# Kernel tuning notes

Hardware: AMD Instinct MI355X
Metric: run time of the kernel (lower is better)

## Reference

```python
import jax, jax.numpy as jnp
import numpy as np

B, S, H = 4, 512, 1024
E, K, I = 8, 2, 2048

def setup_inputs() -> dict:
    key = jax.random.key(0)
    k1, k2, k3, k4, k5 = jax.random.split(key, 5)
    scale_h = 1.0 / np.sqrt(H)
    scale_i = 1.0 / np.sqrt(I)
    return {
        "hidden_states": jax.random.normal(k1, (B, S, H), dtype=jnp.float32),
        "router_w": jax.random.normal(k2, (E, H), dtype=jnp.float32) * scale_h,
        "w_gate": jax.random.normal(k3, (E, H, I), dtype=jnp.float32) * scale_h,
        "w_up": jax.random.normal(k4, (E, H, I), dtype=jnp.float32) * scale_h,
        "w_down": jax.random.normal(k5, (E, I, H), dtype=jnp.float32) * scale_i,
    }

def reference(hidden_states, router_w, w_gate, w_up, w_down):
    b, s, h = hidden_states.shape
    x = hidden_states.reshape(-1, h)              # [T, H] tokens
    T = x.shape[0]

    # ---- RouterTopK: fp32 linear -> softmax over all experts -> top-k ----
    router_logits = x.astype(jnp.float32) @ router_w.T          # [T, E]
    probs = jax.nn.softmax(router_logits, axis=-1)               # [T, E]
    top_vals, top_idx = jax.lax.top_k(probs, K)                  # [T, K]

    # normalize_top_k_affinities (norm_topk_prob=True)
    top_vals = top_vals / jnp.sum(top_vals, axis=-1, keepdims=True)

    # scatter normalized affinities into a dense [T, E] combine matrix
    aff = jnp.zeros((T, E), dtype=x.dtype).at[jnp.arange(T)[:, None], top_idx].set(top_vals.astype(x.dtype))

    # ---- ExpertMLPs: GLU (swiglu) per expert, combine weighted by affinity ----
    # Dense-per-expert computation; non-selected experts contribute 0 via aff.
    gate = jnp.einsum('th,ehi->eti', x, w_gate)                  # [E, T, I]
    up = jnp.einsum('th,ehi->eti', x, w_up)                      # [E, T, I]
    act = jax.nn.silu(gate) * up                                 # [E, T, I]
    expert_out = jnp.einsum('eti,eih->eth', act, w_down)         # [E, T, H]
    out = jnp.einsum('eth,te->th', expert_out, aff)              # [T, H]

    # _reduce_output: all-reduce over TP/world group -> identity single-device
    return out.reshape(b, s, h)
```

## Files before the change

### kernel.cpp

```cpp
#include <hip/hip_runtime.h>
#include <hip/hip_bf16.h>

#define T_TOK 2048
#define H_DIM 1024
#define E_N   8
#define I_DIM 2048

#define NT_MAX 40
#define MAX_SLOTS 5120

typedef unsigned short u16;
typedef unsigned int   u32;
typedef __bf16 bf16_t;
typedef bf16_t bf16x8 __attribute__((ext_vector_type(8)));
typedef u16    u16x8  __attribute__((ext_vector_type(8)));
typedef float  f32x4  __attribute__((ext_vector_type(4)));

#define MFMA __builtin_amdgcn_mfma_f32_16x16x32_bf16

__device__ __forceinline__ u16 bfbits(float f) {
    bf16_t b = (bf16_t)f;
    return __builtin_bit_cast(u16, b);
}

__device__ __forceinline__ int bt_off(int n, int kb) {
    return n * 72 + ((kb ^ ((n >> 2) & 7)) << 3);
}

__global__ __launch_bounds__(64) void router_k(
    const float* __restrict__ x, const float* __restrict__ rw,
    int* __restrict__ cnt, int* __restrict__ tok, float* __restrict__ wts,
    u16* __restrict__ xbf)
{
    int t = blockIdx.x;
    int lane = threadIdx.x;
    const float* xr = x + (size_t)t * H_DIM;
    u16* xbr = xbf + (size_t)t * H_DIM;

    float acc[E_N];
#pragma unroll
    for (int e = 0; e < E_N; e++) acc[e] = 0.f;
    for (int j = 0; j < H_DIM / 64; j++) {
        float xv = xr[lane + 64 * j];
        xbr[lane + 64 * j] = bfbits(xv);
#pragma unroll
        for (int e = 0; e < E_N; e++)
            acc[e] += xv * rw[e * H_DIM + lane + 64 * j];
    }
#pragma unroll
    for (int e = 0; e < E_N; e++) {
        float v = acc[e];
        for (int off = 32; off; off >>= 1) v += __shfl_xor(v, off);
        acc[e] = v;
    }
    if (lane == 0) {
        int i0 = 0; float m0 = acc[0];
#pragma unroll
        for (int e = 1; e < E_N; e++) if (acc[e] > m0) { m0 = acc[e]; i0 = e; }
        int i1 = -1; float m1 = -INFINITY;
#pragma unroll
        for (int e = 0; e < E_N; e++) if (e != i0 && acc[e] > m1) { m1 = acc[e]; i1 = e; }
        float w0 = 1.f / (1.f + expf(m1 - m0));
        float w1 = 1.f - w0;
        int p0 = atomicAdd(&cnt[i0], 1);
        tok[i0 * T_TOK + p0] = t; wts[i0 * T_TOK + p0] = w0;
        int p1 = atomicAdd(&cnt[i1], 1);
        tok[i1 * T_TOK + p1] = t; wts[i1 * T_TOK + p1] = w1;
    }
}

__global__ void prefix_k(const int* __restrict__ cnt, int* __restrict__ offs_pad,
                         int* __restrict__ tile_e, int* __restrict__ tile_row0,
                         int* __restrict__ ntiles)
{
    if (threadIdx.x == 0) {
        int s = 0, nt = 0;
        for (int e = 0; e < E_N; e++) {
            offs_pad[e] = s;
            int c = cnt[e];
            int t = (c + 127) >> 7;
            for (int i = 0; i < t; i++) { tile_e[nt] = e; tile_row0[nt] = i * 128; nt++; }
            s += t * 128;
        }
        offs_pad[E_N] = s;
        *ntiles = nt;
    }
}

__global__ __launch_bounds__(256, 2) void gateup_k(
    const u16* __restrict__ xbf, const float* __restrict__ wg, const float* __restrict__ wu,
    const int* __restrict__ cnt, const int* __restrict__ offs_pad,
    const int* __restrict__ tile_e, const int* __restrict__ tile_row0,
    const int* __restrict__ ntiles, const int* __restrict__ tok,
    u16* __restrict__ act)
{
    int q = gridDim.x >> 3;
    int phys = blockIdx.x;
    int logical = (phys & 7) * q + (phys >> 3);
    int tb = logical % NT_MAX;
    int n0 = (logical / NT_MAX) * 128;
    if (tb >= *ntiles) return;
    int e = tile_e[tb], row0 = tile_row0[tb];
    int cntE = cnt[e];
    int slot0 = offs_pad[e] + row0;

    __shared__ u16 BT[2][2][128 * 72];

    int tid = threadIdx.x;
    int lane = tid & 63, wid = tid >> 6;
    int wm = wid >> 1, wn = wid & 1;
    int l15 = lane & 15, lg = lane >> 4;

    const u16* arow[4];
#pragma unroll
    for (int mf = 0; mf < 4; mf++) {
        int rr = row0 + wm * 64 + mf * 16 + l15;
        int rc = rr < cntE ? rr : cntE - 1;
        arow[mf] = xbf + (size_t)tok[e * T_TOK + rc] * H_DIM;
    }

    int nq = tid & 31;
    int kb = tid >> 5;
    int sn = nq * 4;

    const float* gptr = wg + ((size_t)e * H_DIM + kb * 8) * I_DIM + n0 + sn;
    const float* uptr = wu + ((size_t)e * H_DIM + kb * 8) * I_DIM + n0 + sn;

    float4 vg[8], vu[8];
#pragma unroll
    for (int i = 0; i < 8; i++) {
        vg[i] = *reinterpret_cast<const float4*>(gptr + (size_t)i * I_DIM);
        vu[i] = *reinterpret_cast<const float4*>(uptr + (size_t)i * I_DIM);
    }

    f32x4 accg[4][4], accu[4][4];
#pragma unroll
    for (int a = 0; a < 4; a++)
#pragma unroll
        for (int b = 0; b < 4; b++) { accg[a][b] = (f32x4)0.f; accu[a][b] = (f32x4)0.f; }

    for (int k0 = 0; k0 < H_DIM; k0 += 64) {
        int buf = (k0 >> 6) & 1;
#pragma unroll
        for (int c = 0; c < 4; c++) {
            u16x8 p;
#pragma unroll
            for (int i = 0; i < 8; i++) {
                float f = (c == 0) ? vg[i].x : (c == 1) ? vg[i].y : (c == 2) ? vg[i].z : vg[i].w;
                p[i] = bfbits(f);
            }
            *reinterpret_cast<u16x8*>(&BT[buf][0][bt_off(sn + c, kb)]) = p;
        }
#pragma unroll
        for (int c = 0; c < 4; c++) {
            u16x8 p;
#pragma unroll
            for (int i = 0; i < 8; i++) {
                float f = (c == 0) ? vu[i].x : (c == 1) ? vu[i].y : (c == 2) ? vu[i].z : vu[i].w;
                p[i] = bfbits(f);
            }
            *reinterpret_cast<u16x8*>(&BT[buf][1][bt_off(sn + c, kb)]) = p;
        }
        if (k0 + 64 < H_DIM) {
#pragma unroll
            for (int i = 0; i < 8; i++) {
                vg[i] = *reinterpret_cast<const float4*>(gptr + (size_t)(k0 + 64 + i) * I_DIM);
                vu[i] = *reinterpret_cast<const float4*>(uptr + (size_t)(k0 + 64 + i) * I_DIM);
            }
        }
        __syncthreads();

#pragma unroll
        for (int ks = 0; ks < 2; ks++) {
            bf16x8 af[4];
#pragma unroll
            for (int mf = 0; mf < 4; mf++)
                af[mf] = *reinterpret_cast<const bf16x8*>(arow[mf] + k0 + ks * 32 + lg * 8);
            int kbr = ks * 4 + lg;
#pragma unroll
            for (int nf = 0; nf < 4; nf++) {
                int c = wn * 64 + nf * 16 + l15;
                bf16x8 bg = *reinterpret_cast<const bf16x8*>(&BT[buf][0][bt_off(c, kbr)]);
                bf16x8 bu = *reinterpret_cast<const bf16x8*>(&BT[buf][1][bt_off(c, kbr)]);
#pragma unroll
                for (int mf = 0; mf < 4; mf++) {
                    accg[mf][nf] = MFMA(af[mf], bg, accg[mf][nf], 0, 0, 0);
                    accu[mf][nf] = MFMA(af[mf], bu, accu[mf][nf], 0, 0, 0);
                }
            }
        }
    }

#pragma unroll
    for (int mf = 0; mf < 4; mf++)
#pragma unroll
        for (int j = 0; j < 4; j++) {
            int rl = wm * 64 + mf * 16 + lg * 4 + j;
            bool valid = (row0 + rl) < cntE;
            size_t base = (size_t)(slot0 + rl) * I_DIM + n0;
#pragma unroll
            for (int nf = 0; nf < 4; nf++) {
                float g = accg[mf][nf][j];
                float u = accu[mf][nf][j];
                float a = valid ? (g / (1.f + expf(-g))) * u : 0.f;
                act[base + wn * 64 + nf * 16 + l15] = bfbits(a);
            }
        }
}

__global__ __launch_bounds__(256, 2) void down_k(
    const u16* __restrict__ act, const float* __restrict__ wd,
    const int* __restrict__ cnt, const int* __restrict__ offs_pad,
    const int* __restrict__ tile_e, const int* __restrict__ tile_row0,
    const int* __restrict__ ntiles, const int* __restrict__ tok,
    const float* __restrict__ wts, float* __restrict__ out)
{
    int q = gridDim.x >> 3;
    int phys = blockIdx.x;
    int logical = (phys & 7) * q + (phys >> 3);
    int tb = logical % NT_MAX;
    int h0 = (logical / NT_MAX) * 128;
    if (tb >= *ntiles) return;
    int e = tile_e[tb], row0 = tile_row0[tb];
    int cntE = cnt[e];
    int slot0 = offs_pad[e] + row0;

    __shared__ u16 BT[2][128 * 72];

    int tid = threadIdx.x;
    int lane = tid & 63, wid = tid >> 6;
    int wm = wid >> 1, wn = wid & 1;
    int l15 = lane & 15, lg = lane >> 4;

    const u16* arow[4];
#pragma unroll
    for (int mf = 0; mf < 4; mf++)
        arow[mf] = act + (size_t)(slot0 + wm * 64 + mf * 16 + l15) * I_DIM;

    int nq = tid & 31;
    int kb = tid >> 5;
    int sn = nq * 4;

    const float* dptr = wd + ((size_t)e * I_DIM + kb * 8) * H_DIM + h0 + sn;

    float4 vd[8];
#pragma unroll
    for (int i = 0; i < 8; i++)
        vd[i] = *reinterpret_cast<const float4*>(dptr + (size_t)i * H_DIM);

    f32x4 acc[4][4];
#pragma unroll
    for (int a = 0; a < 4; a++)
#pragma unroll
        for (int b = 0; b < 4; b++) acc[a][b] = (f32x4)0.f;

    for (int k0 = 0; k0 < I_DIM; k0 += 64) {
        int buf = (k0 >> 6) & 1;
#pragma unroll
        for (int c = 0; c < 4; c++) {
            u16x8 p;
#pragma unroll
            for (int i = 0; i < 8; i++) {
                float f = (c == 0) ? vd[i].x : (c == 1) ? vd[i].y : (c == 2) ? vd[i].z : vd[i].w;
                p[i] = bfbits(f);
            }
            *reinterpret_cast<u16x8*>(&BT[buf][bt_off(sn + c, kb)]) = p;
        }
        if (k0 + 64 < I_DIM) {
#pragma unroll
            for (int i = 0; i < 8; i++)
                vd[i] = *reinterpret_cast<const float4*>(dptr + (size_t)(k0 + 64 + i) * H_DIM);
        }
        __syncthreads();

#pragma unroll
        for (int ks = 0; ks < 2; ks++) {
            bf16x8 af[4];
#pragma unroll
            for (int mf = 0; mf < 4; mf++)
                af[mf] = *reinterpret_cast<const bf16x8*>(arow[mf] + k0 + ks * 32 + lg * 8);
            int kbr = ks * 4 + lg;
#pragma unroll
            for (int nf = 0; nf < 4; nf++) {
                int c = wn * 64 + nf * 16 + l15;
                bf16x8 bfr = *reinterpret_cast<const bf16x8*>(&BT[buf][bt_off(c, kbr)]);
#pragma unroll
                for (int mf = 0; mf < 4; mf++)
                    acc[mf][nf] = MFMA(af[mf], bfr, acc[mf][nf], 0, 0, 0);
            }
        }
    }

#pragma unroll
    for (int mf = 0; mf < 4; mf++)
#pragma unroll
        for (int j = 0; j < 4; j++) {
            int rl = wm * 64 + mf * 16 + lg * 4 + j;
            int gr = row0 + rl;
            if (gr < cntE) {
                float w = wts[e * T_TOK + gr];
                int t   = tok[e * T_TOK + gr];
                size_t base = (size_t)t * H_DIM + h0;
#pragma unroll
                for (int nf = 0; nf < 4; nf++)
                    atomicAdd(&out[base + wn * 64 + nf * 16 + l15], acc[mf][nf][j] * w);
            }
        }
}

extern "C" void kernel_launch(void* const* d_in, const int* in_sizes, int n_in,
                              void* d_out, int out_size, void* d_ws, size_t ws_size,
                              hipStream_t stream)
{
    const float* x  = (const float*)d_in[0];
    const float* rw = (const float*)d_in[1];
    const float* wg = (const float*)d_in[2];
    const float* wu = (const float*)d_in[3];
    const float* wd = (const float*)d_in[4];
    float* out = (float*)d_out;

    char* ws = (char*)d_ws;
    int*   cnt       = (int*)(ws);
    int*   ntiles    = (int*)(ws + 32);
    int*   offs_pad  = (int*)(ws + 64);
    int*   tile_e    = (int*)(ws + 256);
    int*   tile_row0 = (int*)(ws + 512);
    int*   tok       = (int*)(ws + 64 * 1024);
    float* wts       = (float*)(ws + 128 * 1024);
    u16*   xbf       = (u16*)(ws + 256 * 1024);
    u16*   act       = (u16*)(ws + 4608 * 1024);

    size_t need = 4608ull * 1024 + (size_t)MAX_SLOTS * I_DIM * 2;
    if (ws_size < need) return;

    hipMemsetAsync(cnt, 0, 32, stream);
    hipMemsetAsync(out, 0, (size_t)T_TOK * H_DIM * sizeof(float), stream);

    router_k<<<T_TOK, 64, 0, stream>>>(x, rw, cnt, tok, wts, xbf);
    prefix_k<<<1, 64, 0, stream>>>(cnt, offs_pad, tile_e, tile_row0, ntiles);
    gateup_k<<<NT_MAX * (I_DIM / 128), 256, 0, stream>>>(
        xbf, wg, wu, cnt, offs_pad, tile_e, tile_row0, ntiles, tok, act);
    down_k<<<NT_MAX * (H_DIM / 128), 256, 0, stream>>>(
        act, wd, cnt, offs_pad, tile_e, tile_row0, ntiles, tok, wts, out);
}
```

Before: 245.7 us.

## Halve GEMM N-tiles and split-K the down projection to raise parallelism

Gate/up GEMM tiles shrink from 128 to 64 output columns, and each half of the block now loads either gate or up weights instead of every thread loading both. The down projection also uses 64-column tiles and splits the K dimension in two, relying on the existing atomicAdd accumulation. Together these give many more blocks, plus higher launch-bounds occupancy hints, to fill the GPU's CUs when expert tiles are few. The cost is more redundant A-operand (activation) reads and twice as many atomic adds to the output.

```diff
diff --git a/kernel.cpp b/kernel.cpp
--- a/kernel.cpp
+++ b/kernel.cpp
@@ -87,7 +87,7 @@
     }
 }
 
-__global__ __launch_bounds__(256, 2) void gateup_k(
+__global__ __launch_bounds__(256, 3) void gateup_k(
     const u16* __restrict__ xbf, const float* __restrict__ wg, const float* __restrict__ wu,
     const int* __restrict__ cnt, const int* __restrict__ offs_pad,
     const int* __restrict__ tile_e, const int* __restrict__ tile_row0,
@@ -98,13 +98,13 @@
     int phys = blockIdx.x;
     int logical = (phys & 7) * q + (phys >> 3);
     int tb = logical % NT_MAX;
-    int n0 = (logical / NT_MAX) * 128;
+    int n0 = (logical / NT_MAX) * 64;
     if (tb >= *ntiles) return;
     int e = tile_e[tb], row0 = tile_row0[tb];
     int cntE = cnt[e];
     int slot0 = offs_pad[e] + row0;
 
-    __shared__ u16 BT[2][2][128 * 72];
+    __shared__ u16 BT[2][2][64 * 72];
 
     int tid = threadIdx.x;
     int lane = tid & 63, wid = tid >> 6;
@@ -119,26 +119,25 @@
         arow[mf] = xbf + (size_t)tok[e * T_TOK + rc] * H_DIM;
     }
 
-    int nq = tid & 31;
-    int kb = tid >> 5;
-    int sn = nq * 4;
-
-    const float* gptr = wg + ((size_t)e * H_DIM + kb * 8) * I_DIM + n0 + sn;
-    const float* uptr = wu + ((size_t)e * H_DIM + kb * 8) * I_DIM + n0 + sn;
-
-    float4 vg[8], vu[8];
-#pragma unroll
-    for (int i = 0; i < 8; i++) {
-        vg[i] = *reinterpret_cast<const float4*>(gptr + (size_t)i * I_DIM);
-        vu[i] = *reinterpret_cast<const float4*>(uptr + (size_t)i * I_DIM);
-    }
-
-    f32x4 accg[4][4], accu[4][4];
+    int mat  = tid >> 7;
+    int tid7 = tid & 127;
+    int kb   = tid7 >> 4;
+    int sn   = (tid7 & 15) * 4;
+
+    const float* wptr = (mat ? wu : wg) + ((size_t)e * H_DIM + kb * 8) * I_DIM + n0 + sn;
+
+    float4 v[8];
+#pragma unroll
+    for (int i = 0; i < 8; i++)
+        v[i] = *reinterpret_cast<const float4*>(wptr + (size_t)i * I_DIM);
+
+    f32x4 accg[4][2], accu[4][2];
 #pragma unroll
     for (int a = 0; a < 4; a++)
 #pragma unroll
-        for (int b = 0; b < 4; b++) { accg[a][b] = (f32x4)0.f; accu[a][b] = (f32x4)0.f; }
-
+        for (int b = 0; b < 2; b++) { accg[a][b] = (f32x4)0.f; accu[a][b] = (f32x4)0.f; }
+
+#pragma unroll 2
     for (int k0 = 0; k0 < H_DIM; k0 += 64) {
         int buf = (k0 >> 6) & 1;
 #pragma unroll
@@ -146,27 +145,15 @@
             u16x8 p;
 #pragma unroll
             for (int i = 0; i < 8; i++) {
-                float f = (c == 0) ? vg[i].x : (c == 1) ? vg[i].y : (c == 2) ? vg[i].z : vg[i].w;
+                float f = (c == 0) ? v[i].x : (c == 1) ? v[i].y : (c == 2) ? v[i].z : v[i].w;
                 p[i] = bfbits(f);
             }
-            *reinterpret_cast<u16x8*>(&BT[buf][0][bt_off(sn + c, kb)]) = p;
-        }
-#pragma unroll
-        for (int c = 0; c < 4; c++) {
-            u16x8 p;
-#pragma unroll
-            for (int i = 0; i < 8; i++) {
-                float f = (c == 0) ? vu[i].x : (c == 1) ? vu[i].y : (c == 2) ? vu[i].z : vu[i].w;
-                p[i] = bfbits(f);
-            }
-            *reinterpret_cast<u16x8*>(&BT[buf][1][bt_off(sn + c, kb)]) = p;
+            *reinterpret_cast<u16x8*>(&BT[buf][mat][bt_off(sn + c, kb)]) = p;
         }
         if (k0 + 64 < H_DIM) {
 #pragma unroll
-            for (int i = 0; i < 8; i++) {
-                vg[i] = *reinterpret_cast<const float4*>(gptr + (size_t)(k0 + 64 + i) * I_DIM);
-                vu[i] = *reinterpret_cast<const float4*>(uptr + (size_t)(k0 + 64 + i) * I_DIM);
-            }
+            for (int i = 0; i < 8; i++)
+                v[i] = *reinterpret_cast<const float4*>(wptr + (size_t)(k0 + 64 + i) * I_DIM);
         }
         __syncthreads();
 
@@ -178,8 +165,8 @@
                 af[mf] = *reinterpret_cast<const bf16x8*>(arow[mf] + k0 + ks * 32 + lg * 8);
             int kbr = ks * 4 + lg;
 #pragma unroll
-            for (int nf = 0; nf < 4; nf++) {
-                int c = wn * 64 + nf * 16 + l15;
+            for (int nf = 0; nf < 2; nf++) {
+                int c = wn * 32 + nf * 16 + l15;
                 bf16x8 bg = *reinterpret_cast<const bf16x8*>(&BT[buf][0][bt_off(c, kbr)]);
                 bf16x8 bu = *reinterpret_cast<const bf16x8*>(&BT[buf][1][bt_off(c, kbr)]);
 #pragma unroll
@@ -199,16 +186,16 @@
             bool valid = (row0 + rl) < cntE;
             size_t base = (size_t)(slot0 + rl) * I_DIM + n0;
 #pragma unroll
-            for (int nf = 0; nf < 4; nf++) {
+            for (int nf = 0; nf < 2; nf++) {
                 float g = accg[mf][nf][j];
                 float u = accu[mf][nf][j];
                 float a = valid ? (g / (1.f + expf(-g))) * u : 0.f;
-                act[base + wn * 64 + nf * 16 + l15] = bfbits(a);
-            }
-        }
-}
-
-__global__ __launch_bounds__(256, 2) void down_k(
+                act[base + wn * 32 + nf * 16 + l15] = bfbits(a);
+            }
+        }
+}
+
+__global__ __launch_bounds__(256, 4) void down_k(
     const u16* __restrict__ act, const float* __restrict__ wd,
     const int* __restrict__ cnt, const int* __restrict__ offs_pad,
     const int* __restrict__ tile_e, const int* __restrict__ tile_row0,
@@ -219,13 +206,15 @@
     int phys = blockIdx.x;
     int logical = (phys & 7) * q + (phys >> 3);
     int tb = logical % NT_MAX;
-    int h0 = (logical / NT_MAX) * 128;
+    int rest = logical / NT_MAX;
+    int h0 = (rest & 15) * 64;
+    int kh = rest >> 4;
     if (tb >= *ntiles) return;
     int e = tile_e[tb], row0 = tile_row0[tb];
     int cntE = cnt[e];
     int slot0 = offs_pad[e] + row0;
 
-    __shared__ u16 BT[2][128 * 72];
+    __shared__ u16 BT[2][64 * 72];
 
     int tid = threadIdx.x;
     int lane = tid & 63, wid = tid >> 6;
@@ -235,41 +224,39 @@
     const u16* arow[4];
 #pragma unroll
     for (int mf = 0; mf < 4; mf++)
-        arow[mf] = act + (size_t)(slot0 + wm * 64 + mf * 16 + l15) * I_DIM;
-
-    int nq = tid & 31;
+        arow[mf] = act + (size_t)(slot0 + wm * 64 + mf * 16 + l15) * I_DIM + kh * 1024;
+
     int kb = tid >> 5;
-    int sn = nq * 4;
-
-    const float* dptr = wd + ((size_t)e * I_DIM + kb * 8) * H_DIM + h0 + sn;
-
-    float4 vd[8];
+    int sn = (tid & 31) * 2;
+
+    const float* dptr = wd + ((size_t)e * I_DIM + kh * 1024 + kb * 8) * H_DIM + h0 + sn;
+
+    float2 v[8];
 #pragma unroll
     for (int i = 0; i < 8; i++)
-        vd[i] = *reinterpret_cast<const float4*>(dptr + (size_t)i * H_DIM);
-
-    f32x4 acc[4][4];
+        v[i] = *reinterpret_cast<const float2*>(dptr + (size_t)i * H_DIM);
+
+    f32x4 acc[4][2];
 #pragma unroll
     for (int a = 0; a < 4; a++)
 #pragma unroll
-        for (int b = 0; b < 4; b++) acc[a][b] = (f32x4)0.f;
-
-    for (int k0 = 0; k0 < I_DIM; k0 += 64) {
+        for (int b = 0; b < 2; b++) acc[a][b] = (f32x4)0.f;
+
+#pragma unroll 2
+    for (int k0 = 0; k0 < 1024; k0 += 64) {
         int buf = (k0 >> 6) & 1;
 #pragma unroll
-        for (int c = 0; c < 4; c++) {
+        for (int c = 0; c < 2; c++) {
             u16x8 p;
 #pragma unroll
-            for (int i = 0; i < 8; i++) {
-                float f = (c == 0) ? vd[i].x : (c == 1) ? vd[i].y : (c == 2) ? vd[i].z : vd[i].w;
-                p[i] = bfbits(f);
-            }
+            for (int i = 0; i < 8; i++)
+                p[i] = bfbits(c ? v[i].y : v[i].x);
             *reinterpret_cast<u16x8*>(&BT[buf][bt_off(sn + c, kb)]) = p;
         }
-        if (k0 + 64 < I_DIM) {
+        if (k0 + 64 < 1024) {
 #pragma unroll
             for (int i = 0; i < 8; i++)
-                vd[i] = *reinterpret_cast<const float4*>(dptr + (size_t)(k0 + 64 + i) * H_DIM);
+                v[i] = *reinterpret_cast<const float2*>(dptr + (size_t)(k0 + 64 + i) * H_DIM);
         }
         __syncthreads();
 
@@ -281,8 +268,8 @@
                 af[mf] = *reinterpret_cast<const bf16x8*>(arow[mf] + k0 + ks * 32 + lg * 8);
             int kbr = ks * 4 + lg;
 #pragma unroll
-            for (int nf = 0; nf < 4; nf++) {
-                int c = wn * 64 + nf * 16 + l15;
+            for (int nf = 0; nf < 2; nf++) {
+                int c = wn * 32 + nf * 16 + l15;
                 bf16x8 bfr = *reinterpret_cast<const bf16x8*>(&BT[buf][bt_off(c, kbr)]);
 #pragma unroll
                 for (int mf = 0; mf < 4; mf++)
@@ -302,8 +289,8 @@
                 int t   = tok[e * T_TOK + gr];
                 size_t base = (size_t)t * H_DIM + h0;
 #pragma unroll
-                for (int nf = 0; nf < 4; nf++)
-                    atomicAdd(&out[base + wn * 64 + nf * 16 + l15], acc[mf][nf][j] * w);
+                for (int nf = 0; nf < 2; nf++)
+                    atomicAdd(&out[base + wn * 32 + nf * 16 + l15], acc[mf][nf][j] * w);
             }
         }
 }
@@ -338,8 +325,8 @@
 
     router_k<<<T_TOK, 64, 0, stream>>>(x, rw, cnt, tok, wts, xbf);
     prefix_k<<<1, 64, 0, stream>>>(cnt, offs_pad, tile_e, tile_row0, ntiles);
-    gateup_k<<<NT_MAX * (I_DIM / 128), 256, 0, stream>>>(
+    gateup_k<<<NT_MAX * (I_DIM / 64), 256, 0, stream>>>(
         xbf, wg, wu, cnt, offs_pad, tile_e, tile_row0, ntiles, tok, act);
-    down_k<<<NT_MAX * (H_DIM / 128), 256, 0, stream>>>(
+    down_k<<<NT_MAX * (H_DIM / 64) * 2, 256, 0, stream>>>(
         act, wd, cnt, offs_pad, tile_e, tile_row0, ntiles, tok, wts, out);
 }
```

New measurement: 273.2 us. +11.2%, slower.

## Restructure gate/up and down GEMM prefetch pipeline and split-K the down projection

Applied to the files above, without the earlier changes.

Both GEMM kernels now preload the first weight tile into shared memory before the loop. Inside the loop they issue the next global loads right after the barrier, run the MFMAs, and only then convert and store the next tile into the alternate buffer, so global latency overlaps compute. The down kernel also splits its K dimension into two halves across twice as many blocks, relying on the existing atomicAdd epilogue, and raises its launch-bounds occupancy hint to 3. Split-K doubles the atomic traffic to the output and rereads routing metadata, and the tighter occupancy target may cause register spills.

```diff
diff --git a/kernel.cpp b/kernel.cpp
--- a/kernel.cpp
+++ b/kernel.cpp
@@ -132,6 +132,18 @@
         vg[i] = *reinterpret_cast<const float4*>(gptr + (size_t)i * I_DIM);
         vu[i] = *reinterpret_cast<const float4*>(uptr + (size_t)i * I_DIM);
     }
+#pragma unroll
+    for (int c = 0; c < 4; c++) {
+        u16x8 pg, pu;
+#pragma unroll
+        for (int i = 0; i < 8; i++) {
+            float fg = (c == 0) ? vg[i].x : (c == 1) ? vg[i].y : (c == 2) ? vg[i].z : vg[i].w;
+            float fu = (c == 0) ? vu[i].x : (c == 1) ? vu[i].y : (c == 2) ? vu[i].z : vu[i].w;
+            pg[i] = bfbits(fg); pu[i] = bfbits(fu);
+        }
+        *reinterpret_cast<u16x8*>(&BT[0][0][bt_off(sn + c, kb)]) = pg;
+        *reinterpret_cast<u16x8*>(&BT[0][1][bt_off(sn + c, kb)]) = pu;
+    }
 
     f32x4 accg[4][4], accu[4][4];
 #pragma unroll
@@ -139,36 +151,20 @@
 #pragma unroll
         for (int b = 0; b < 4; b++) { accg[a][b] = (f32x4)0.f; accu[a][b] = (f32x4)0.f; }
 
+#pragma unroll 2
     for (int k0 = 0; k0 < H_DIM; k0 += 64) {
         int buf = (k0 >> 6) & 1;
-#pragma unroll
-        for (int c = 0; c < 4; c++) {
-            u16x8 p;
-#pragma unroll
-            for (int i = 0; i < 8; i++) {
-                float f = (c == 0) ? vg[i].x : (c == 1) ? vg[i].y : (c == 2) ? vg[i].z : vg[i].w;
-                p[i] = bfbits(f);
-            }
-            *reinterpret_cast<u16x8*>(&BT[buf][0][bt_off(sn + c, kb)]) = p;
-        }
-#pragma unroll
-        for (int c = 0; c < 4; c++) {
-            u16x8 p;
-#pragma unroll
-            for (int i = 0; i < 8; i++) {
-                float f = (c == 0) ? vu[i].x : (c == 1) ? vu[i].y : (c == 2) ? vu[i].z : vu[i].w;
-                p[i] = bfbits(f);
-            }
-            *reinterpret_cast<u16x8*>(&BT[buf][1][bt_off(sn + c, kb)]) = p;
-        }
-        if (k0 + 64 < H_DIM) {
+        bool more = (k0 + 64) < H_DIM;
+
+        __syncthreads();
+
+        if (more) {
 #pragma unroll
             for (int i = 0; i < 8; i++) {
                 vg[i] = *reinterpret_cast<const float4*>(gptr + (size_t)(k0 + 64 + i) * I_DIM);
                 vu[i] = *reinterpret_cast<const float4*>(uptr + (size_t)(k0 + 64 + i) * I_DIM);
             }
         }
-        __syncthreads();
 
 #pragma unroll
         for (int ks = 0; ks < 2; ks++) {
@@ -187,6 +183,21 @@
                     accg[mf][nf] = MFMA(af[mf], bg, accg[mf][nf], 0, 0, 0);
                     accu[mf][nf] = MFMA(af[mf], bu, accu[mf][nf], 0, 0, 0);
                 }
+            }
+        }
+
+        if (more) {
+#pragma unroll
+            for (int c = 0; c < 4; c++) {
+                u16x8 pg, pu;
+#pragma unroll
+                for (int i = 0; i < 8; i++) {
+                    float fg = (c == 0) ? vg[i].x : (c == 1) ? vg[i].y : (c == 2) ? vg[i].z : vg[i].w;
+                    float fu = (c == 0) ? vu[i].x : (c == 1) ? vu[i].y : (c == 2) ? vu[i].z : vu[i].w;
+                    pg[i] = bfbits(fg); pu[i] = bfbits(fu);
+                }
+                *reinterpret_cast<u16x8*>(&BT[buf ^ 1][0][bt_off(sn + c, kb)]) = pg;
+                *reinterpret_cast<u16x8*>(&BT[buf ^ 1][1][bt_off(sn + c, kb)]) = pu;
             }
         }
     }
@@ -208,7 +219,7 @@
         }
 }
 
-__global__ __launch_bounds__(256, 2) void down_k(
+__global__ __launch_bounds__(256, 3) void down_k(
     const u16* __restrict__ act, const float* __restrict__ wd,
     const int* __restrict__ cnt, const int* __restrict__ offs_pad,
     const int* __restrict__ tile_e, const int* __restrict__ tile_row0,
@@ -219,7 +230,9 @@
     int phys = blockIdx.x;
     int logical = (phys & 7) * q + (phys >> 3);
     int tb = logical % NT_MAX;
-    int h0 = (logical / NT_MAX) * 128;
+    int rest = logical / NT_MAX;
+    int h0 = (rest & 7) * 128;
+    int kh = rest >> 3;
     if (tb >= *ntiles) return;
     int e = tile_e[tb], row0 = tile_row0[tb];
     int cntE = cnt[e];
@@ -235,18 +248,27 @@
     const u16* arow[4];
 #pragma unroll
     for (int mf = 0; mf < 4; mf++)
-        arow[mf] = act + (size_t)(slot0 + wm * 64 + mf * 16 + l15) * I_DIM;
-
-    int nq = tid & 31;
+        arow[mf] = act + (size_t)(slot0 + wm * 64 + mf * 16 + l15) * I_DIM + kh * 1024;
+
     int kb = tid >> 5;
-    int sn = nq * 4;
-
-    const float* dptr = wd + ((size_t)e * I_DIM + kb * 8) * H_DIM + h0 + sn;
-
-    float4 vd[8];
+    int sn = (tid & 31) * 4;
+
+    const float* dptr = wd + ((size_t)e * I_DIM + kh * 1024 + kb * 8) * H_DIM + h0 + sn;
+
+    float4 v[8];
 #pragma unroll
     for (int i = 0; i < 8; i++)
-        vd[i] = *reinterpret_cast<const float4*>(dptr + (size_t)i * H_DIM);
+        v[i] = *reinterpret_cast<const float4*>(dptr + (size_t)i * H_DIM);
+#pragma unroll
+    for (int c = 0; c < 4; c++) {
+        u16x8 p;
+#pragma unroll
+        for (int i = 0; i < 8; i++) {
+            float f = (c == 0) ? v[i].x : (c == 1) ? v[i].y : (c == 2) ? v[i].z : v[i].w;
+            p[i] = bfbits(f);
+        }
+        *reinterpret_cast<u16x8*>(&BT[0][bt_off(sn + c, kb)]) = p;
+    }
 
     f32x4 acc[4][4];
 #pragma unroll
@@ -254,24 +276,18 @@
 #pragma unroll
         for (int b = 0; b < 4; b++) acc[a][b] = (f32x4)0.f;
 
-    for (int k0 = 0; k0 < I_DIM; k0 += 64) {
+#pragma unroll 2
+    for (int k0 = 0; k0 < 1024; k0 += 64) {
         int buf = (k0 >> 6) & 1;
-#pragma unroll
-        for (int c = 0; c < 4; c++) {
-            u16x8 p;
-#pragma unroll
-            for (int i = 0; i < 8; i++) {
-                float f = (c == 0) ? vd[i].x : (c == 1) ? vd[i].y : (c == 2) ? vd[i].z : vd[i].w;
-                p[i] = bfbits(f);
-            }
-            *reinterpret_cast<u16x8*>(&BT[buf][bt_off(sn + c, kb)]) = p;
-        }
-        if (k0 + 64 < I_DIM) {
+        bool more = (k0 + 64) < 1024;
+
+        __syncthreads();
+
+        if (more) {
 #pragma unroll
             for (int i = 0; i < 8; i++)
-                vd[i] = *reinterpret_cast<const float4*>(dptr + (size_t)(k0 + 64 + i) * H_DIM);
-        }
-        __syncthreads();
+                v[i] = *reinterpret_cast<const float4*>(dptr + (size_t)(k0 + 64 + i) * H_DIM);
+        }
 
 #pragma unroll
         for (int ks = 0; ks < 2; ks++) {
@@ -287,6 +303,19 @@
 #pragma unroll
                 for (int mf = 0; mf < 4; mf++)
                     acc[mf][nf] = MFMA(af[mf], bfr, acc[mf][nf], 0, 0, 0);
+            }
+        }
+
+        if (more) {
+#pragma unroll
+            for (int c = 0; c < 4; c++) {
+                u16x8 p;
+#pragma unroll
+                for (int i = 0; i < 8; i++) {
+                    float f = (c == 0) ? v[i].x : (c == 1) ? v[i].y : (c == 2) ? v[i].z : v[i].w;
+                    p[i] = bfbits(f);
+                }
+                *reinterpret_cast<u16x8*>(&BT[buf ^ 1][bt_off(sn + c, kb)]) = p;
             }
         }
     }
@@ -340,6 +369,6 @@
     prefix_k<<<1, 64, 0, stream>>>(cnt, offs_pad, tile_e, tile_row0, ntiles);
     gateup_k<<<NT_MAX * (I_DIM / 128), 256, 0, stream>>>(
         xbf, wg, wu, cnt, offs_pad, tile_e, tile_row0, ntiles, tok, act);
-    down_k<<<NT_MAX * (H_DIM / 128), 256, 0, stream>>>(
+    down_k<<<NT_MAX * (H_DIM / 128) * 2, 256, 0, stream>>>(
         act, wd, cnt, offs_pad, tile_e, tile_row0, ntiles, tok, wts, out);
 }
```

New measurement: 319.3 us. +29.9%, slower.

## Pre-convert expert weights to swizzled bf16 tiles and stream via global_load_lds

Applied to the files above, without the earlier changes.

Adds a conversion kernel that transposes all gate, up and down weights to bf16 and packs them into LDS-ready swizzled 128x64 tiles in workspace. New gate/up and down kernels then copy those tiles straight into LDS with global_load_lds, with no per-tile fp32 loads or in-register conversion. The down kernel also splits K in two and accumulates with atomics to get more blocks and occupancy. The conversion reads every weight each call and writes a bf16 copy, which adds traffic. A fallback path is kept when the workspace is too small.

```diff
diff --git a/kernel.cpp b/kernel.cpp
--- a/kernel.cpp
+++ b/kernel.cpp
@@ -21,6 +21,16 @@
 __device__ __forceinline__ u16 bfbits(float f) {
     bf16_t b = (bf16_t)f;
     return __builtin_bit_cast(u16, b);
+}
+
+__device__ __forceinline__ void gload_lds16(const void* g, void* l) {
+    __builtin_amdgcn_global_load_lds(
+        (const __attribute__((address_space(1))) void*)g,
+        (__attribute__((address_space(3))) void*)l, 16, 0, 0);
+}
+
+__device__ __forceinline__ int tile_off(int n, int kb) {
+    return n * 64 + ((kb ^ ((n >> 1) & 7)) << 3);
 }
 
 __device__ __forceinline__ int bt_off(int n, int kb) {
@@ -87,7 +97,242 @@
     }
 }
 
-__global__ __launch_bounds__(256, 2) void gateup_k(
+__global__ __launch_bounds__(256) void cvtw_k(
+    const float* __restrict__ wg, const float* __restrict__ wu, const float* __restrict__ wd,
+    u16* __restrict__ tg, u16* __restrict__ tu, u16* __restrict__ td)
+{
+    __shared__ float S[64][132];
+    int bid = blockIdx.x;
+    int kind = bid >> 11;
+    int ti = bid & 2047;
+    const float* src; u16* dst; int nstr;
+    if (kind < 2) {
+        const float* w = kind ? wu : wg;
+        int e = ti >> 8, b = ti & 15;
+        int p = (ti >> 4) & 15;
+        src = w + ((size_t)e * H_DIM + b * 64) * I_DIM + p * 128;
+        nstr = I_DIM;
+        dst = (kind ? tu : tg) + (size_t)ti * 8192;
+    } else {
+        int e = ti >> 8, r = ti & 255;
+        int p = r >> 5, b = r & 31;
+        src = wd + ((size_t)e * I_DIM + b * 64) * H_DIM + p * 128;
+        nstr = H_DIM;
+        dst = td + (size_t)ti * 8192;
+    }
+    int t = threadIdx.x;
+#pragma unroll
+    for (int i = 0; i < 8; i++) {
+        int idx = t + i * 256;
+        int k = idx >> 5, c4 = idx & 31;
+        float4 v = *reinterpret_cast<const float4*>(src + (size_t)k * nstr + c4 * 4);
+        *reinterpret_cast<float4*>(&S[k][c4 * 4]) = v;
+    }
+    __syncthreads();
+#pragma unroll
+    for (int i = 0; i < 4; i++) {
+        int oidx = t + i * 256;
+        int n = oidx & 127, kb = oidx >> 7;
+        u16x8 pk;
+#pragma unroll
+        for (int j = 0; j < 8; j++) pk[j] = bfbits(S[kb * 8 + j][n]);
+        *reinterpret_cast<u16x8*>(dst + tile_off(n, kb)) = pk;
+    }
+}
+
+__global__ __launch_bounds__(256, 2) void gateupA_k(
+    const u16* __restrict__ xbf, const u16* __restrict__ tg, const u16* __restrict__ tu,
+    const int* __restrict__ cnt, const int* __restrict__ offs_pad,
+    const int* __restrict__ tile_e, const int* __restrict__ tile_row0,
+    const int* __restrict__ ntiles, const int* __restrict__ tok,
+    u16* __restrict__ act)
+{
+    int q = gridDim.x >> 3;
+    int phys = blockIdx.x;
+    int logical = (phys & 7) * q + (phys >> 3);
+    int tb = logical % NT_MAX;
+    int p  = logical / NT_MAX;
+    if (tb >= *ntiles) return;
+    int e = tile_e[tb], row0 = tile_row0[tb];
+    int cntE = cnt[e];
+    int slot0 = offs_pad[e] + row0;
+    int n0 = p * 128;
+
+    __shared__ u16 BT[2][2][8192];
+
+    int tid = threadIdx.x;
+    int lane = tid & 63, wid = tid >> 6;
+    int wm = wid >> 1, wn = wid & 1;
+    int l15 = lane & 15, lg = lane >> 4;
+
+    const u16* arow[4];
+#pragma unroll
+    for (int mf = 0; mf < 4; mf++) {
+        int rr = row0 + wm * 64 + mf * 16 + l15;
+        int rc = rr < cntE ? rr : cntE - 1;
+        arow[mf] = xbf + (size_t)tok[e * T_TOK + rc] * H_DIM;
+    }
+
+    const u16* tgB = tg + ((size_t)(e * 16 + p) * 16) * 8192;
+    const u16* tuB = tu + ((size_t)(e * 16 + p) * 16) * 8192;
+
+#define STAGE_GU(bufi, b) { \
+    const u16* gG = tgB + (size_t)(b) * 8192; \
+    const u16* gU = tuB + (size_t)(b) * 8192; \
+    _Pragma("unroll") \
+    for (int i_ = 0; i_ < 4; i_++) { \
+        int ub = i_ * 256 + wid * 64; \
+        gload_lds16(gG + (ub + lane) * 8, &BT[bufi][0][ub * 8]); \
+        gload_lds16(gU + (ub + lane) * 8, &BT[bufi][1][ub * 8]); \
+    } }
+
+    f32x4 accg[4][4], accu[4][4];
+#pragma unroll
+    for (int a = 0; a < 4; a++)
+#pragma unroll
+        for (int b = 0; b < 4; b++) { accg[a][b] = (f32x4)0.f; accu[a][b] = (f32x4)0.f; }
+
+    STAGE_GU(0, 0);
+    __syncthreads();
+
+    for (int b = 0; b < 16; b++) {
+        int buf = b & 1;
+        if (b + 1 < 16) STAGE_GU(buf ^ 1, b + 1);
+
+#pragma unroll
+        for (int ks = 0; ks < 2; ks++) {
+            bf16x8 af[4];
+#pragma unroll
+            for (int mf = 0; mf < 4; mf++)
+                af[mf] = *reinterpret_cast<const bf16x8*>(arow[mf] + b * 64 + ks * 32 + lg * 8);
+            int kbr = ks * 4 + lg;
+#pragma unroll
+            for (int nf = 0; nf < 4; nf++) {
+                int c = wn * 64 + nf * 16 + l15;
+                int o = tile_off(c, kbr);
+                bf16x8 bg = *reinterpret_cast<const bf16x8*>(&BT[buf][0][o]);
+                bf16x8 bu = *reinterpret_cast<const bf16x8*>(&BT[buf][1][o]);
+#pragma unroll
+                for (int mf = 0; mf < 4; mf++) {
+                    accg[mf][nf] = MFMA(af[mf], bg, accg[mf][nf], 0, 0, 0);
+                    accu[mf][nf] = MFMA(af[mf], bu, accu[mf][nf], 0, 0, 0);
+                }
+            }
+        }
+        __syncthreads();
+    }
+
+#pragma unroll
+    for (int mf = 0; mf < 4; mf++)
+#pragma unroll
+        for (int j = 0; j < 4; j++) {
+            int rl = wm * 64 + mf * 16 + lg * 4 + j;
+            bool valid = (row0 + rl) < cntE;
+            size_t base = (size_t)(slot0 + rl) * I_DIM + n0;
+#pragma unroll
+            for (int nf = 0; nf < 4; nf++) {
+                float g = accg[mf][nf][j];
+                float u = accu[mf][nf][j];
+                float a = valid ? (g / (1.f + expf(-g))) * u : 0.f;
+                act[base + wn * 64 + nf * 16 + l15] = bfbits(a);
+            }
+        }
+#undef STAGE_GU
+}
+
+__global__ __launch_bounds__(256, 3) void downA_k(
+    const u16* __restrict__ act, const u16* __restrict__ td,
+    const int* __restrict__ cnt, const int* __restrict__ offs_pad,
+    const int* __restrict__ tile_e, const int* __restrict__ tile_row0,
+    const int* __restrict__ ntiles, const int* __restrict__ tok,
+    const float* __restrict__ wts, float* __restrict__ out)
+{
+    int q = gridDim.x >> 3;
+    int phys = blockIdx.x;
+    int logical = (phys & 7) * q + (phys >> 3);
+    int tb = logical % NT_MAX;
+    int rest = logical / NT_MAX;
+    int p  = rest & 7;
+    int kh = rest >> 3;
+    if (tb >= *ntiles) return;
+    int e = tile_e[tb], row0 = tile_row0[tb];
+    int cntE = cnt[e];
+    int slot0 = offs_pad[e] + row0;
+    int h0 = p * 128;
+
+    __shared__ u16 BT[2][8192];
+
+    int tid = threadIdx.x;
+    int lane = tid & 63, wid = tid >> 6;
+    int wm = wid >> 1, wn = wid & 1;
+    int l15 = lane & 15, lg = lane >> 4;
+
+    const u16* arow[4];
+#pragma unroll
+    for (int mf = 0; mf < 4; mf++)
+        arow[mf] = act + (size_t)(slot0 + wm * 64 + mf * 16 + l15) * I_DIM + kh * 1024;
+
+    const u16* tdB = td + ((size_t)(e * 8 + p) * 32 + kh * 16) * 8192;
+
+#define STAGE_D(bufi, b) { \
+    const u16* gD = tdB + (size_t)(b) * 8192; \
+    _Pragma("unroll") \
+    for (int i_ = 0; i_ < 4; i_++) { \
+        int ub = i_ * 256 + wid * 64; \
+        gload_lds16(gD + (ub + lane) * 8, &BT[bufi][ub * 8]); \
+    } }
+
+    f32x4 acc[4][4];
+#pragma unroll
+    for (int a = 0; a < 4; a++)
+#pragma unroll
+        for (int b = 0; b < 4; b++) acc[a][b] = (f32x4)0.f;
+
+    STAGE_D(0, 0);
+    __syncthreads();
+
+    for (int b = 0; b < 16; b++) {
+        int buf = b & 1;
+        if (b + 1 < 16) STAGE_D(buf ^ 1, b + 1);
+
+#pragma unroll
+        for (int ks = 0; ks < 2; ks++) {
+            bf16x8 af[4];
+#pragma unroll
+            for (int mf = 0; mf < 4; mf++)
+                af[mf] = *reinterpret_cast<const bf16x8*>(arow[mf] + b * 64 + ks * 32 + lg * 8);
+            int kbr = ks * 4 + lg;
+#pragma unroll
+            for (int nf = 0; nf < 4; nf++) {
+                int c = wn * 64 + nf * 16 + l15;
+                bf16x8 bd = *reinterpret_cast<const bf16x8*>(&BT[buf][tile_off(c, kbr)]);
+#pragma unroll
+                for (int mf = 0; mf < 4; mf++)
+                    acc[mf][nf] = MFMA(af[mf], bd, acc[mf][nf], 0, 0, 0);
+            }
+        }
+        __syncthreads();
+    }
+
+#pragma unroll
+    for (int mf = 0; mf < 4; mf++)
+#pragma unroll
+        for (int j = 0; j < 4; j++) {
+            int rl = wm * 64 + mf * 16 + lg * 4 + j;
+            int gr = row0 + rl;
+            if (gr < cntE) {
+                float w = wts[e * T_TOK + gr];
+                int t   = tok[e * T_TOK + gr];
+                size_t base = (size_t)t * H_DIM + h0;
+#pragma unroll
+                for (int nf = 0; nf < 4; nf++)
+                    atomicAdd(&out[base + wn * 64 + nf * 16 + l15], acc[mf][nf][j] * w);
+            }
+        }
+#undef STAGE_D
+}
+
+__global__ __launch_bounds__(256, 2) void gateupB_k(
     const u16* __restrict__ xbf, const float* __restrict__ wg, const float* __restrict__ wu,
     const int* __restrict__ cnt, const int* __restrict__ offs_pad,
     const int* __restrict__ tile_e, const int* __restrict__ tile_row0,
@@ -143,23 +388,15 @@
         int buf = (k0 >> 6) & 1;
 #pragma unroll
         for (int c = 0; c < 4; c++) {
-            u16x8 p;
+            u16x8 pg, pu;
 #pragma unroll
             for (int i = 0; i < 8; i++) {
-                float f = (c == 0) ? vg[i].x : (c == 1) ? vg[i].y : (c == 2) ? vg[i].z : vg[i].w;
-                p[i] = bfbits(f);
-            }
-            *reinterpret_cast<u16x8*>(&BT[buf][0][bt_off(sn + c, kb)]) = p;
-        }
-#pragma unroll
-        for (int c = 0; c < 4; c++) {
-            u16x8 p;
-#pragma unroll
-            for (int i = 0; i < 8; i++) {
-                float f = (c == 0) ? vu[i].x : (c == 1) ? vu[i].y : (c == 2) ? vu[i].z : vu[i].w;
-                p[i] = bfbits(f);
-            }
-            *reinterpret_cast<u16x8*>(&BT[buf][1][bt_off(sn + c, kb)]) = p;
+                float fg = (c == 0) ? vg[i].x : (c == 1) ? vg[i].y : (c == 2) ? vg[i].z : vg[i].w;
+                float fu = (c == 0) ? vu[i].x : (c == 1) ? vu[i].y : (c == 2) ? vu[i].z : vu[i].w;
+                pg[i] = bfbits(fg); pu[i] = bfbits(fu);
+            }
+            *reinterpret_cast<u16x8*>(&BT[buf][0][bt_off(sn + c, kb)]) = pg;
+            *reinterpret_cast<u16x8*>(&BT[buf][1][bt_off(sn + c, kb)]) = pu;
         }
         if (k0 + 64 < H_DIM) {
 #pragma unroll
@@ -208,7 +445,7 @@
         }
 }
 
-__global__ __launch_bounds__(256, 2) void down_k(
+__global__ __launch_bounds__(256, 2) void downB_k(
     const u16* __restrict__ act, const float* __restrict__ wd,
     const int* __restrict__ cnt, const int* __restrict__ offs_pad,
     const int* __restrict__ tile_e, const int* __restrict__ tile_row0,
@@ -237,16 +474,15 @@
     for (int mf = 0; mf < 4; mf++)
         arow[mf] = act + (size_t)(slot0 + wm * 64 + mf * 16 + l15) * I_DIM;
 
-    int nq = tid & 31;
     int kb = tid >> 5;
-    int sn = nq * 4;
+    int sn = (tid & 31) * 4;
 
     const float* dptr = wd + ((size_t)e * I_DIM + kb * 8) * H_DIM + h0 + sn;
 
-    float4 vd[8];
+    float4 v[8];
 #pragma unroll
     for (int i = 0; i < 8; i++)
-        vd[i] = *reinterpret_cast<const float4*>(dptr + (size_t)i * H_DIM);
+        v[i] = *reinterpret_cast<const float4*>(dptr + (size_t)i * H_DIM);
 
     f32x4 acc[4][4];
 #pragma unroll
@@ -261,7 +497,7 @@
             u16x8 p;
 #pragma unroll
             for (int i = 0; i < 8; i++) {
-                float f = (c == 0) ? vd[i].x : (c == 1) ? vd[i].y : (c == 2) ? vd[i].z : vd[i].w;
+                float f = (c == 0) ? v[i].x : (c == 1) ? v[i].y : (c == 2) ? v[i].z : v[i].w;
                 p[i] = bfbits(f);
             }
             *reinterpret_cast<u16x8*>(&BT[buf][bt_off(sn + c, kb)]) = p;
@@ -269,7 +505,7 @@
         if (k0 + 64 < I_DIM) {
 #pragma unroll
             for (int i = 0; i < 8; i++)
-                vd[i] = *reinterpret_cast<const float4*>(dptr + (size_t)(k0 + 64 + i) * H_DIM);
+                v[i] = *reinterpret_cast<const float4*>(dptr + (size_t)(k0 + 64 + i) * H_DIM);
         }
         __syncthreads();
 
@@ -330,16 +566,33 @@
     u16*   xbf       = (u16*)(ws + 256 * 1024);
     u16*   act       = (u16*)(ws + 4608 * 1024);
 
-    size_t need = 4608ull * 1024 + (size_t)MAX_SLOTS * I_DIM * 2;
-    if (ws_size < need) return;
+    const size_t OFF_TG = 28ull << 20;
+    const size_t TSZ    = 2048ull * 16384;
+    u16* tg = (u16*)(ws + OFF_TG);
+    u16* tu = (u16*)(ws + OFF_TG + TSZ);
+    u16* td = (u16*)(ws + OFF_TG + 2 * TSZ);
+
+    size_t need_b = 4608ull * 1024 + (size_t)MAX_SLOTS * I_DIM * 2;
+    size_t need_a = OFF_TG + 3 * TSZ;
+    if (ws_size < need_b) return;
+    bool big = ws_size >= need_a;
 
     hipMemsetAsync(cnt, 0, 32, stream);
     hipMemsetAsync(out, 0, (size_t)T_TOK * H_DIM * sizeof(float), stream);
 
     router_k<<<T_TOK, 64, 0, stream>>>(x, rw, cnt, tok, wts, xbf);
     prefix_k<<<1, 64, 0, stream>>>(cnt, offs_pad, tile_e, tile_row0, ntiles);
-    gateup_k<<<NT_MAX * (I_DIM / 128), 256, 0, stream>>>(
-        xbf, wg, wu, cnt, offs_pad, tile_e, tile_row0, ntiles, tok, act);
-    down_k<<<NT_MAX * (H_DIM / 128), 256, 0, stream>>>(
-        act, wd, cnt, offs_pad, tile_e, tile_row0, ntiles, tok, wts, out);
-}
+
+    if (big) {
+        cvtw_k<<<3 * 2048, 256, 0, stream>>>(wg, wu, wd, tg, tu, td);
+        gateupA_k<<<NT_MAX * (I_DIM / 128), 256, 0, stream>>>(
+            xbf, tg, tu, cnt, offs_pad, tile_e, tile_row0, ntiles, tok, act);
+        downA_k<<<NT_MAX * (H_DIM / 128) * 2, 256, 0, stream>>>(
+            act, td, cnt, offs_pad, tile_e, tile_row0, ntiles, tok, wts, out);
+    } else {
+        gateupB_k<<<NT_MAX * (I_DIM / 128), 256, 0, stream>>>(
+            xbf, wg, wu, cnt, offs_pad, tile_e, tile_row0, ntiles, tok, act);
+        downB_k<<<NT_MAX * (H_DIM / 128), 256, 0, stream>>>(
+            act, wd, cnt, offs_pad, tile_e, tile_row0, ntiles, tok, wts, out);
+    }
+}
```

After: 274.6 us. 1.12x slower.
